# Kernel tuning notes

Hardware: AMD Instinct MI355X
Metric: run time of the kernel (lower is better)

Reference implementation:

```python
import jax, jax.numpy as jnp
import numpy as np

OUT, IN = 11008, 4096
B, S = 8, 64

def setup_inputs() -> dict:
    key = jax.random.key(0)
    k1, k2, k3, k4 = jax.random.split(key, 4)
    x = jax.random.normal(k1, (B, S, IN), dtype=jnp.float32)
    # symmetric int8 values in [-127, 127]
    q_weight = jax.random.randint(k2, (OUT, IN), -127, 128, dtype=jnp.int32)
    # positive per-row scales, small like real quant scales
    scale = jax.random.uniform(k3, (OUT, 1), dtype=jnp.float32, minval=1e-4, maxval=2e-2)
    bias = jax.random.normal(k4, (OUT,), dtype=jnp.float32)
    return {"x": x, "q_weight": q_weight, "scale": scale, "bias": bias}

def reference(x, q_weight, scale, bias):
    # Dequantize per output row, then dense matmul (F.linear: y = x @ W.T + b)
    weight = (q_weight.astype(jnp.float32) * scale).astype(x.dtype)  # [OUT, IN]
    return jnp.einsum('bsi,oi->bso', x, weight) + bias.astype(x.dtype)
```

## Files before the change

### kernel.cpp

```cpp
#include <hip/hip_runtime.h>
#include <stdint.h>

#define M_TOK 512
#define N_OUT 11008
#define K_IN  4096
#define BM 512
#define BN 64
#define BKS 256
#define NSPAN (K_IN / BKS)

typedef int i32x4 __attribute__((ext_vector_type(4)));

__global__ void xquant_kernel(const float* __restrict__ x, int8_t* __restrict__ x8f,
                              float* __restrict__ sx) {
  const int row = blockIdx.x * 4 + (threadIdx.x >> 6);
  const int lane = threadIdx.x & 63;
  const float4* xr = (const float4*)(x + (size_t)row * K_IN);

  float4 v[16];
  float m = 0.f;
#pragma unroll
  for (int j = 0; j < 16; ++j) {
    v[j] = xr[lane * 16 + j];
    m = fmaxf(m, fmaxf(fmaxf(fabsf(v[j].x), fabsf(v[j].y)),
                       fmaxf(fabsf(v[j].z), fabsf(v[j].w))));
  }
#pragma unroll
  for (int o = 32; o; o >>= 1) m = fmaxf(m, __shfl_xor(m, o));

  const float inv = 127.0f / m;
  if (lane == 0) sx[row] = m / 127.0f;

  uint32_t d[16];
#pragma unroll
  for (int j = 0; j < 16; ++j) {
    int a = __float2int_rn(v[j].x * inv);
    int b = __float2int_rn(v[j].y * inv);
    int c = __float2int_rn(v[j].z * inv);
    int e = __float2int_rn(v[j].w * inv);
    d[j] = (a & 0xFF) | ((b & 0xFF) << 8) | ((c & 0xFF) << 16) | (e << 24);
  }
  const int gm = row >> 4, mr = row & 15;
#pragma unroll
  for (int q = 0; q < 4; ++q) {
    const int kc16 = lane * 4 + q;
    *(uint4*)&x8f[(size_t)(kc16 * 32 + gm) * 256 + mr * 16] =
        make_uint4(d[4 * q], d[4 * q + 1], d[4 * q + 2], d[4 * q + 3]);
  }
}

__global__ __launch_bounds__(1024, 4)
void qgemm_i8(const int8_t* __restrict__ x8f, const float* __restrict__ sx,
              const int* __restrict__ qw, const float* __restrict__ scale,
              const float* __restrict__ bias, float* __restrict__ out) {
  __shared__ __align__(16) int8_t Bs[2][BN * BKS];

  const int tid = threadIdx.x;
  const int lane = tid & 63;
  const int wm = tid >> 6;
  const int kc = lane >> 4;

  const int bn0 = blockIdx.x * BN;
  const int gmbase = wm * 2;

  i32x4 acc[2][4] = {};
  i32x4 aS[8];
  int4 br[4];

  const int brow = tid >> 4;
  const int bq = tid & 15;

#define LGKM_BAR() asm volatile("s_waitcnt lgkmcnt(0)\ns_barrier" ::: "memory")

#define A_ISSUE_ALL(k0)                                                          \
  {                                                                              \
    const int kbase16 = (k0) >> 4;                                               \
    _Pragma("unroll") for (int kk = 0; kk < 4; ++kk) {                           \
      _Pragma("unroll") for (int mi = 0; mi < 2; ++mi) {                         \
        aS[kk * 2 + mi] =                                                        \
            *(const i32x4*)&x8f[(size_t)((kbase16 + kk * 4 + kc) * 32 + gmbase + mi) * 256 + \
                                (lane & 15) * 16];                               \
      }                                                                          \
    }                                                                            \
  }

#define B_ISSUE(k0)                                                              \
  {                                                                              \
    const int4* bp = (const int4*)(qw + (size_t)(bn0 + brow) * K_IN + (k0) + bq * 16); \
    _Pragma("unroll") for (int k = 0; k < 4; ++k) br[k] = bp[k];                 \
  }

#define B_WRITE(BI)                                                              \
  {                                                                              \
    uint32_t d[4];                                                               \
    _Pragma("unroll") for (int k = 0; k < 4; ++k) {                              \
      int4 w = br[k];                                                            \
      uint32_t lo = __builtin_amdgcn_perm((uint32_t)w.y, (uint32_t)w.x, 0x0C0C0400u); \
      uint32_t hi = __builtin_amdgcn_perm((uint32_t)w.w, (uint32_t)w.z, 0x04000C0Cu); \
      d[k] = lo | hi;                                                            \
    }                                                                            \
    const int ch = bq ^ (brow & 15);                                             \
    *(uint4*)&Bs[BI][brow * 256 + ch * 16] = make_uint4(d[0], d[1], d[2], d[3]); \
  }

#define COMPUTE(BI)                                                              \
  {                                                                              \
    _Pragma("unroll") for (int kk = 0; kk < 4; ++kk) {                           \
      i32x4 b[4];                                                                \
      _Pragma("unroll") for (int ni = 0; ni < 4; ++ni) {                         \
        const int row = ni * 16 + (lane & 15);                                   \
        const int ch = (kk * 4 + kc) ^ (row & 15);                               \
        b[ni] = *(const i32x4*)&Bs[BI][row * 256 + ch * 16];                     \
      }                                                                          \
      __builtin_amdgcn_s_setprio(1);                                             \
      _Pragma("unroll") for (int mi = 0; mi < 2; ++mi)                           \
        _Pragma("unroll") for (int ni = 0; ni < 4; ++ni)                         \
          acc[mi][ni] = __builtin_amdgcn_mfma_i32_16x16x64_i8(aS[kk * 2 + mi], b[ni], \
                                                              acc[mi][ni], 0, 0, 0); \
      __builtin_amdgcn_s_setprio(0);                                             \
    }                                                                            \
  }

  B_ISSUE(0);
  A_ISSUE_ALL(0);
  B_WRITE(0);
  B_ISSUE(BKS);
  LGKM_BAR();

#pragma unroll 1
  for (int t = 0; t < NSPAN; ++t) {
    const int cur = t & 1;
    if (t + 1 < NSPAN) B_WRITE(cur ^ 1);
    if (t + 2 < NSPAN) B_ISSUE((t + 2) * BKS);

    COMPUTE(cur);

    if (t + 1 < NSPAN) {
      A_ISSUE_ALL((t + 1) * BKS);
      LGKM_BAR();
    }
  }

  float sxr[2][4];
#pragma unroll
  for (int mi = 0; mi < 2; ++mi)
#pragma unroll
    for (int r = 0; r < 4; ++r)
      sxr[mi][r] = sx[wm * 32 + mi * 16 + (lane >> 4) * 4 + r];

#pragma unroll
  for (int ni = 0; ni < 4; ++ni) {
    const int col = bn0 + ni * 16 + (lane & 15);
    const float sw = scale[col];
    const float bi = bias[col];
#pragma unroll
    for (int mi = 0; mi < 2; ++mi) {
      const int rowb = wm * 32 + mi * 16 + (lane >> 4) * 4;
#pragma unroll
      for (int r = 0; r < 4; ++r) {
        out[(size_t)(rowb + r) * N_OUT + col] = (float)acc[mi][ni][r] * sxr[mi][r] * sw + bi;
      }
    }
  }
#undef LGKM_BAR
#undef A_ISSUE_ALL
#undef B_ISSUE
#undef B_WRITE
#undef COMPUTE
}

__global__ void qgemm_naive(const float* __restrict__ x, const int* __restrict__ qw,
                            const float* __restrict__ scale, const float* __restrict__ bias,
                            float* __restrict__ out) {
  int o = blockIdx.x * blockDim.x + threadIdx.x;
  if (o >= M_TOK * N_OUT) return;
  int row = o / N_OUT, col = o % N_OUT;
  const float* xr = x + (size_t)row * K_IN;
  const int* wr = qw + (size_t)col * K_IN;
  float acc = 0.f;
  for (int k = 0; k < K_IN; ++k) acc += xr[k] * (float)wr[k];
  out[o] = acc * scale[col] + bias[col];
}

extern "C" void kernel_launch(void* const* d_in, const int* in_sizes, int n_in,
                              void* d_out, int out_size, void* d_ws, size_t ws_size,
                              hipStream_t stream) {
  const float* x = (const float*)d_in[0];
  const int* qw = (const int*)d_in[1];
  const float* scale = (const float*)d_in[2];
  const float* bias = (const float*)d_in[3];
  float* out = (float*)d_out;

  const size_t sx_bytes = 4096;
  const size_t x8_bytes = (size_t)M_TOK * K_IN;

  if (ws_size >= sx_bytes + x8_bytes) {
    float* sx = (float*)d_ws;
    int8_t* x8f = (int8_t*)((char*)d_ws + sx_bytes);
    xquant_kernel<<<dim3(M_TOK / 4), dim3(256), 0, stream>>>(x, x8f, sx);
    qgemm_i8<<<dim3(N_OUT / BN), dim3(1024), 0, stream>>>(x8f, sx, qw, scale, bias, out);
  } else {
    qgemm_naive<<<dim3((M_TOK * N_OUT + 255) / 256), dim3(256), 0, stream>>>(
        x, qw, scale, bias, out);
  }
}
```

Measured before the change: 60.43 us.

## Double K-span per barrier and split each span into two pipelined halves

```diff
diff --git a/kernel.cpp b/kernel.cpp
--- a/kernel.cpp
+++ b/kernel.cpp
@@ -6,7 +6,8 @@
 #define K_IN  4096
 #define BM 512
 #define BN 64
-#define BKS 256
+#define BKS 512
+#define HK  256
 #define NSPAN (K_IN / BKS)
 
 typedef int i32x4 __attribute__((ext_vector_type(4)));
@@ -72,7 +73,7 @@
 
 #define LGKM_BAR() asm volatile("s_waitcnt lgkmcnt(0)\ns_barrier" ::: "memory")
 
-#define A_ISSUE_ALL(k0)                                                          \
+#define A_ISSUE_H(k0)                                                            \
   {                                                                              \
     const int kbase16 = (k0) >> 4;                                               \
     _Pragma("unroll") for (int kk = 0; kk < 4; ++kk) {                           \
@@ -90,7 +91,7 @@
     _Pragma("unroll") for (int k = 0; k < 4; ++k) br[k] = bp[k];                 \
   }
 
-#define B_WRITE(BI)                                                              \
+#define B_WRITE_H(BI, h)                                                         \
   {                                                                              \
     uint32_t d[4];                                                               \
     _Pragma("unroll") for (int k = 0; k < 4; ++k) {                              \
@@ -99,44 +100,50 @@
       uint32_t hi = __builtin_amdgcn_perm((uint32_t)w.w, (uint32_t)w.z, 0x04000C0Cu); \
       d[k] = lo | hi;                                                            \
     }                                                                            \
-    const int ch = bq ^ (brow & 15);                                             \
-    *(uint4*)&Bs[BI][brow * 256 + ch * 16] = make_uint4(d[0], d[1], d[2], d[3]); \
-  }
-
-#define COMPUTE(BI)                                                              \
-  {                                                                              \
+    const int ch = (h) * 16 + (bq ^ (brow & 15));                                \
+    *(uint4*)&Bs[BI][brow * 512 + ch * 16] = make_uint4(d[0], d[1], d[2], d[3]); \
+  }
+
+#define COMPUTE_H(BI, h)                                                         \
+  {                                                                              \
+    __builtin_amdgcn_s_setprio(1);                                               \
     _Pragma("unroll") for (int kk = 0; kk < 4; ++kk) {                           \
       i32x4 b[4];                                                                \
       _Pragma("unroll") for (int ni = 0; ni < 4; ++ni) {                         \
         const int row = ni * 16 + (lane & 15);                                   \
-        const int ch = (kk * 4 + kc) ^ (row & 15);                               \
-        b[ni] = *(const i32x4*)&Bs[BI][row * 256 + ch * 16];                     \
+        const int ch = (h) * 16 + ((kk * 4 + kc) ^ (row & 15));                  \
+        b[ni] = *(const i32x4*)&Bs[BI][row * 512 + ch * 16];                     \
       }                                                                          \
-      __builtin_amdgcn_s_setprio(1);                                             \
       _Pragma("unroll") for (int mi = 0; mi < 2; ++mi)                           \
         _Pragma("unroll") for (int ni = 0; ni < 4; ++ni)                         \
           acc[mi][ni] = __builtin_amdgcn_mfma_i32_16x16x64_i8(aS[kk * 2 + mi], b[ni], \
                                                               acc[mi][ni], 0, 0, 0); \
-      __builtin_amdgcn_s_setprio(0);                                             \
     }                                                                            \
+    __builtin_amdgcn_s_setprio(0);                                               \
   }
 
   B_ISSUE(0);
-  A_ISSUE_ALL(0);
-  B_WRITE(0);
+  A_ISSUE_H(0);
+  B_WRITE_H(0, 0);
+  B_ISSUE(HK);
+  B_WRITE_H(0, 1);
   B_ISSUE(BKS);
   LGKM_BAR();
 
 #pragma unroll 1
   for (int t = 0; t < NSPAN; ++t) {
     const int cur = t & 1;
-    if (t + 1 < NSPAN) B_WRITE(cur ^ 1);
+    const int nxt = cur ^ 1;
+
+    if (t + 1 < NSPAN) B_WRITE_H(nxt, 0);
+    if (t + 1 < NSPAN) B_ISSUE((t + 1) * BKS + HK);
+    COMPUTE_H(cur, 0);
+    A_ISSUE_H(t * BKS + HK);
+    if (t + 1 < NSPAN) B_WRITE_H(nxt, 1);
     if (t + 2 < NSPAN) B_ISSUE((t + 2) * BKS);
-
-    COMPUTE(cur);
-
+    COMPUTE_H(cur, 1);
     if (t + 1 < NSPAN) {
-      A_ISSUE_ALL((t + 1) * BKS);
+      A_ISSUE_H((t + 1) * BKS);
       LGKM_BAR();
     }
   }
@@ -163,10 +170,10 @@
     }
   }
 #undef LGKM_BAR
-#undef A_ISSUE_ALL
+#undef A_ISSUE_H
 #undef B_ISSUE
-#undef B_WRITE
-#undef COMPUTE
+#undef B_WRITE_H
+#undef COMPUTE_H
 }
 
 __global__ void qgemm_naive(const float* __restrict__ x, const int* __restrict__ qw,
```

After: 64.15 us. +6.2%, slower.
